# Performance work log

Hardware: AMD Instinct MI355X
Metric: run time of the kernel (lower is better)

Reference implementation:

```python
import jax, jax.numpy as jnp
import numpy as np

N, M, D = 8192, 8192, 64


def setup_inputs() -> dict:
    key = jax.random.key(0)
    k1, k2 = jax.random.split(key)
    return {
        "x": jax.random.normal(k1, (N, D), dtype=jnp.float32),
        "y": jax.random.normal(k2, (M, D), dtype=jnp.float32),
        "log_lengthscale": jnp.zeros((D,), dtype=jnp.float32),
        "log_outputscale": jnp.zeros((1,), dtype=jnp.float32),
    }


def reference(x, y, log_lengthscale, log_outputscale):
    # ARD RBF: k(x,y) = outputscale * exp(-0.5 * sum_d ((x_d - y_d)/l_d)^2)
    lengthscale = jnp.exp(log_lengthscale)          # [D]
    outputscale = jnp.exp(log_outputscale)          # [1]
    xs = x / lengthscale                            # [N, D]
    ys = y / lengthscale                            # [M, D]
    # ||xs - ys||^2 = ||xs||^2 + ||ys||^2 - 2 xs.ys^T  (GEMM rewrite, same math)
    x2 = jnp.sum(xs * xs, axis=-1)                  # [N]
    y2 = jnp.sum(ys * ys, axis=-1)                  # [M]
    cross = jnp.einsum("nd,md->nm", xs, ys)         # [N, M]
    sq_dist = jnp.maximum(x2[:, None] + y2[None, :] - 2.0 * cross, 0.0)
    return outputscale * jnp.exp(-0.5 * sq_dist)    # [N, M]
```

## Files before the change

kernel.cpp:

```cpp
#include <hip/hip_runtime.h>
#include <hip/hip_bf16.h>

#define NROWS 8192
#define MCOLS 8192
#define DDIM  64

typedef __attribute__((ext_vector_type(8))) short bf16x8;
typedef __attribute__((ext_vector_type(4))) float f32x4;
typedef __attribute__((ext_vector_type(2))) unsigned int u32x2;
typedef __attribute__((ext_vector_type(4))) unsigned int u32x4;

#define WS_NEED (4ull * 1024 * 1024 + 64 * 1024)

__global__ __launch_bounds__(256)
void pack_kernel(const float* __restrict__ x, const float* __restrict__ y,
                 const float* __restrict__ log_l, unsigned char* __restrict__ ws)
{
    const int t = threadIdx.x, lane = t & 63, wid = t >> 6;
    const int sub = lane & 15, lg = lane >> 4;
    const int gb  = blockIdx.x;
    const int isY = gb >> 7;
    const int rb  = ((gb & 127) << 2) | wid;

    const float* __restrict__ src = isY ? y : x;
    bf16x8* __restrict__ Ph = reinterpret_cast<bf16x8*>(ws + (isY ? (2u << 20) : 0u));
    bf16x8* __restrict__ Pl = reinterpret_cast<bf16x8*>(ws + (isY ? (3u << 20) : (1u << 20)));
    float*  __restrict__ nrm = reinterpret_cast<float*>(ws + (4u << 20) + (isY ? (32u << 10) : 0u));

    const int row = rb * 16 + sub;
    float psum = 0.0f;
    #pragma unroll
    for (int kk = 0; kk < 2; ++kk) {
        const int k0 = kk * 32 + lg * 8;
        f32x4 v0 = *reinterpret_cast<const f32x4*>(&src[(size_t)row * DDIM + k0]);
        f32x4 v1 = *reinterpret_cast<const f32x4*>(&src[(size_t)row * DDIM + k0 + 4]);
        f32x4 g0 = *reinterpret_cast<const f32x4*>(&log_l[k0]);
        f32x4 g1 = *reinterpret_cast<const f32x4*>(&log_l[k0 + 4]);
        float s[8];
        #pragma unroll
        for (int j = 0; j < 4; ++j) s[j]     = v0[j] * __expf(-g0[j]);
        #pragma unroll
        for (int j = 0; j < 4; ++j) s[4 + j] = v1[j] * __expf(-g1[j]);
        unsigned int hp[4], lp[4];
        #pragma unroll
        for (int p = 0; p < 4; ++p) {
            float a = s[2 * p], b = s[2 * p + 1];
            psum += a * a + b * b;
            unsigned int ua = __float_as_uint(a), ub = __float_as_uint(b);
            float la = a - __uint_as_float(ua & 0xFFFF0000u);
            float lb = b - __uint_as_float(ub & 0xFFFF0000u);
            hp[p] = (ua >> 16) | (ub & 0xFFFF0000u);
            lp[p] = ((__float_as_uint(la) + 0x8000u) >> 16) |
                    ((__float_as_uint(lb) + 0x8000u) & 0xFFFF0000u);
        }
        const int fi = (rb * 2 + kk) * 64 + lane;
        *reinterpret_cast<u32x4*>(&Ph[fi]) = u32x4{hp[0], hp[1], hp[2], hp[3]};
        *reinterpret_cast<u32x4*>(&Pl[fi]) = u32x4{lp[0], lp[1], lp[2], lp[3]};
    }
    psum += __shfl_xor(psum, 16);
    psum += __shfl_xor(psum, 32);
    if (lg == 0) nrm[row] = psum;
}

__global__ __launch_bounds__(256, 4)
void ard_rbf_main(const unsigned char* __restrict__ ws,
                  const float* __restrict__ log_os, float* __restrict__ out)
{
    __shared__ float lds[4][32][68];

    const int t = threadIdx.x, lane = t & 63, wid = t >> 6;
    const int sub = lane & 15, lg = lane >> 4;
    const int bx = blockIdx.x;
    const int by = blockIdx.y;

    const bf16x8* __restrict__ Xh = reinterpret_cast<const bf16x8*>(ws);
    const bf16x8* __restrict__ Xl = reinterpret_cast<const bf16x8*>(ws + (1u << 20));
    const bf16x8* __restrict__ Yh = reinterpret_cast<const bf16x8*>(ws + (2u << 20));
    const bf16x8* __restrict__ Yl = reinterpret_cast<const bf16x8*>(ws + (3u << 20));
    const float*  __restrict__ x2 = reinterpret_cast<const float*>(ws + (4u << 20));
    const float*  __restrict__ y2 = reinterpret_cast<const float*>(ws + (4u << 20) + (32u << 10));

    const int xrb = by * 8 + wid * 2;
    const int yrb = bx * 4;

    f32x4 acc[2][4] = {};
    #pragma unroll
    for (int kk = 0; kk < 2; ++kk) {
        bf16x8 xh[2], xl[2], yh[4], yl[4];
        #pragma unroll
        for (int a = 0; a < 2; ++a) {
            const int fi = ((xrb + a) * 2 + kk) * 64 + lane;
            xh[a] = Xh[fi];
            xl[a] = Xl[fi];
        }
        #pragma unroll
        for (int b = 0; b < 4; ++b) {
            const int fj = ((yrb + b) * 2 + kk) * 64 + lane;
            yh[b] = Yh[fj];
            yl[b] = Yl[fj];
        }
        #pragma unroll
        for (int a = 0; a < 2; ++a)
            #pragma unroll
            for (int b = 0; b < 4; ++b) {
                acc[a][b] = __builtin_amdgcn_mfma_f32_16x16x32_bf16(yh[b], xh[a], acc[a][b], 0, 0, 0);
                acc[a][b] = __builtin_amdgcn_mfma_f32_16x16x32_bf16(yl[b], xh[a], acc[a][b], 0, 0, 0);
                acc[a][b] = __builtin_amdgcn_mfma_f32_16x16x32_bf16(yh[b], xl[a], acc[a][b], 0, 0, 0);
            }
    }

    #pragma unroll
    for (int a = 0; a < 2; ++a)
        #pragma unroll
        for (int b = 0; b < 4; ++b)
            *reinterpret_cast<f32x4*>(&lds[wid][a * 16 + sub][b * 16 + lg * 4]) = acc[a][b];

    const float lnos = log_os[0];
    const int xbase = by * 128 + wid * 32;
    const int ybase = bx * 64;
    const f32x4 y2q = *reinterpret_cast<const f32x4*>(&y2[ybase + sub * 4]);

    #pragma unroll
    for (int r = 0; r < 8; ++r) {
        const int rloc = r * 4 + lg;
        f32x4 c = *reinterpret_cast<const f32x4*>(&lds[wid][rloc][sub * 4]);
        const float xs = x2[xbase + rloc];
        f32x4 v;
        #pragma unroll
        for (int j = 0; j < 4; ++j) {
            float sq = fmaxf(xs + y2q[j] - 2.0f * c[j], 0.0f);
            v[j] = __expf(fmaf(-0.5f, sq, lnos));
        }
        *reinterpret_cast<f32x4*>(out + (size_t)(xbase + rloc) * MCOLS + ybase + sub * 4) = v;
    }
}

__global__ __launch_bounds__(512, 4)
void ard_rbf_fallback(const float* __restrict__ x, const float* __restrict__ y,
                      const float* __restrict__ log_l, const float* __restrict__ log_os,
                      float* __restrict__ out)
{
    __shared__ unsigned short Ah[128][DDIM + 8], Al[128][DDIM + 8];
    __shared__ unsigned short Bh[128][DDIM + 8], Bl[128][DDIM + 8];
    __shared__ float x2s[128], y2s[128];
    __shared__ float invl[DDIM];

    const int t = threadIdx.x;
    const int bx = blockIdx.x, by = blockIdx.y;
    const int lane = t & 63, sub = lane & 15, lg = lane >> 4;

    if (t < DDIM) invl[t] = __expf(-log_l[t]);
    __syncthreads();

    #pragma unroll
    for (int ab = 0; ab < 2; ++ab) {
        const float* __restrict__ src = ab ? y : x;
        unsigned short (*Hh)[DDIM + 8] = ab ? Bh : Ah;
        unsigned short (*Hl)[DDIM + 8] = ab ? Bl : Al;
        float* nrm = ab ? y2s : x2s;
        const int tb = (ab ? bx : by) * 128;
        #pragma unroll
        for (int i = 0; i < 4; ++i) {
            const int f = i * 512 + t;
            const int row = f >> 4;
            const int c4 = (f & 15) * 4;
            f32x4 v = *reinterpret_cast<const f32x4*>(&src[(size_t)(tb + row) * DDIM + c4]);
            f32x4 il = *reinterpret_cast<const f32x4*>(&invl[c4]);
            float s0 = v[0] * il[0], s1 = v[1] * il[1], s2 = v[2] * il[2], s3 = v[3] * il[3];
            float psum = s0 * s0 + s1 * s1 + s2 * s2 + s3 * s3;
            unsigned int u0 = __float_as_uint(s0), u1 = __float_as_uint(s1);
            unsigned int u2 = __float_as_uint(s2), u3 = __float_as_uint(s3);
            float l0 = s0 - __uint_as_float(u0 & 0xFFFF0000u);
            float l1 = s1 - __uint_as_float(u1 & 0xFFFF0000u);
            float l2 = s2 - __uint_as_float(u2 & 0xFFFF0000u);
            float l3 = s3 - __uint_as_float(u3 & 0xFFFF0000u);
            unsigned int hp0 = (u0 >> 16) | (u1 & 0xFFFF0000u);
            unsigned int hp1 = (u2 >> 16) | (u3 & 0xFFFF0000u);
            unsigned int lp0 = ((__float_as_uint(l0) + 0x8000u) >> 16) | ((__float_as_uint(l1) + 0x8000u) & 0xFFFF0000u);
            unsigned int lp1 = ((__float_as_uint(l2) + 0x8000u) >> 16) | ((__float_as_uint(l3) + 0x8000u) & 0xFFFF0000u);
            psum += __shfl_xor(psum, 1);
            psum += __shfl_xor(psum, 2);
            psum += __shfl_xor(psum, 4);
            psum += __shfl_xor(psum, 8);
            *reinterpret_cast<u32x2*>(&Hh[row][c4]) = u32x2{hp0, hp1};
            *reinterpret_cast<u32x2*>(&Hl[row][c4]) = u32x2{lp0, lp1};
            if (sub == 0) nrm[row] = psum;
        }
    }
    __syncthreads();

    const int wid = t >> 6;
    const int wr = wid >> 2, wc = wid & 3;
    f32x4 acc[4][2] = {};
    #pragma unroll
    for (int kk = 0; kk < 2; ++kk) {
        const int kb = kk * 32 + lg * 8;
        bf16x8 ah[4], al[4];
        #pragma unroll
        for (int m = 0; m < 4; ++m) {
            const int r = wr * 64 + m * 16 + sub;
            ah[m] = *reinterpret_cast<const bf16x8*>(&Ah[r][kb]);
            al[m] = *reinterpret_cast<const bf16x8*>(&Al[r][kb]);
        }
        #pragma unroll
        for (int n = 0; n < 2; ++n) {
            const int c = wc * 32 + n * 16 + sub;
            bf16x8 bh = *reinterpret_cast<const bf16x8*>(&Bh[c][kb]);
            bf16x8 bl = *reinterpret_cast<const bf16x8*>(&Bl[c][kb]);
            #pragma unroll
            for (int m = 0; m < 4; ++m) {
                acc[m][n] = __builtin_amdgcn_mfma_f32_16x16x32_bf16(ah[m], bh, acc[m][n], 0, 0, 0);
                acc[m][n] = __builtin_amdgcn_mfma_f32_16x16x32_bf16(al[m], bh, acc[m][n], 0, 0, 0);
                acc[m][n] = __builtin_amdgcn_mfma_f32_16x16x32_bf16(ah[m], bl, acc[m][n], 0, 0, 0);
            }
        }
    }
    const float lnos = log_os[0];
    #pragma unroll
    for (int m = 0; m < 4; ++m) {
        const int rl0 = wr * 64 + m * 16 + lg * 4;
        #pragma unroll
        for (int n = 0; n < 2; ++n) {
            const int cl = wc * 32 + n * 16 + sub;
            const float yy2 = y2s[cl];
            const size_t g0 = (size_t)(by * 128 + rl0) * MCOLS + (size_t)(bx * 128 + cl);
            #pragma unroll
            for (int j = 0; j < 4; ++j) {
                float sq = fmaxf(x2s[rl0 + j] + yy2 - 2.0f * acc[m][n][j], 0.0f);
                out[g0 + (size_t)j * MCOLS] = __expf(fmaf(-0.5f, sq, lnos));
            }
        }
    }
}

extern "C" void kernel_launch(void* const* d_in, const int* in_sizes, int n_in,
                              void* d_out, int out_size, void* d_ws, size_t ws_size,
                              hipStream_t stream) {
    const float* x      = (const float*)d_in[0];
    const float* y      = (const float*)d_in[1];
    const float* log_l  = (const float*)d_in[2];
    const float* log_os = (const float*)d_in[3];
    float* out = (float*)d_out;

    if (ws_size >= WS_NEED) {
        pack_kernel<<<256, 256, 0, stream>>>(x, y, log_l, (unsigned char*)d_ws);
        ard_rbf_main<<<dim3(128, 64), 256, 0, stream>>>((const unsigned char*)d_ws, log_os, out);
    } else {
        ard_rbf_fallback<<<dim3(64, 64), 512, 0, stream>>>(x, y, log_l, log_os, out);
    }
}
```

Before: 63.17 us.

## Stage Y tile in LDS via global_load_lds and loop over four X tiles per block

```diff
diff --git a/kernel.cpp b/kernel.cpp
--- a/kernel.cpp
+++ b/kernel.cpp
@@ -11,6 +11,12 @@
 typedef __attribute__((ext_vector_type(4))) unsigned int u32x4;
 
 #define WS_NEED (4ull * 1024 * 1024 + 64 * 1024)
+
+__device__ __forceinline__ void gld_lds16(const unsigned char* g, unsigned char* l) {
+    __builtin_amdgcn_global_load_lds(
+        (const __attribute__((address_space(1))) void*)g,
+        (__attribute__((address_space(3))) void*)l, 16, 0, 0);
+}
 
 __global__ __launch_bounds__(256)
 void pack_kernel(const float* __restrict__ x, const float* __restrict__ y,
@@ -62,76 +68,86 @@
     if (lg == 0) nrm[row] = psum;
 }
 
-__global__ __launch_bounds__(256, 4)
+__global__ __launch_bounds__(256, 3)
 void ard_rbf_main(const unsigned char* __restrict__ ws,
                   const float* __restrict__ log_os, float* __restrict__ out)
 {
-    __shared__ float lds[4][32][68];
+    __shared__ __align__(1024) unsigned char smemY[16 * 1024];
+    __shared__ float tr[4][16][68];
 
     const int t = threadIdx.x, lane = t & 63, wid = t >> 6;
     const int sub = lane & 15, lg = lane >> 4;
     const int bx = blockIdx.x;
-    const int by = blockIdx.y;
+    const int g  = blockIdx.y;
 
     const bf16x8* __restrict__ Xh = reinterpret_cast<const bf16x8*>(ws);
     const bf16x8* __restrict__ Xl = reinterpret_cast<const bf16x8*>(ws + (1u << 20));
-    const bf16x8* __restrict__ Yh = reinterpret_cast<const bf16x8*>(ws + (2u << 20));
-    const bf16x8* __restrict__ Yl = reinterpret_cast<const bf16x8*>(ws + (3u << 20));
     const float*  __restrict__ x2 = reinterpret_cast<const float*>(ws + (4u << 20));
     const float*  __restrict__ y2 = reinterpret_cast<const float*>(ws + (4u << 20) + (32u << 10));
 
-    const int xrb = by * 8 + wid * 2;
-    const int yrb = bx * 4;
-
-    f32x4 acc[2][4] = {};
-    #pragma unroll
-    for (int kk = 0; kk < 2; ++kk) {
-        bf16x8 xh[2], xl[2], yh[4], yl[4];
-        #pragma unroll
-        for (int a = 0; a < 2; ++a) {
-            const int fi = ((xrb + a) * 2 + kk) * 64 + lane;
-            xh[a] = Xh[fi];
-            xl[a] = Xl[fi];
-        }
-        #pragma unroll
-        for (int b = 0; b < 4; ++b) {
-            const int fj = ((yrb + b) * 2 + kk) * 64 + lane;
-            yh[b] = Yh[fj];
-            yl[b] = Yl[fj];
-        }
-        #pragma unroll
-        for (int a = 0; a < 2; ++a)
-            #pragma unroll
-            for (int b = 0; b < 4; ++b) {
-                acc[a][b] = __builtin_amdgcn_mfma_f32_16x16x32_bf16(yh[b], xh[a], acc[a][b], 0, 0, 0);
-                acc[a][b] = __builtin_amdgcn_mfma_f32_16x16x32_bf16(yl[b], xh[a], acc[a][b], 0, 0, 0);
-                acc[a][b] = __builtin_amdgcn_mfma_f32_16x16x32_bf16(yh[b], xl[a], acc[a][b], 0, 0, 0);
-            }
-    }
-
-    #pragma unroll
-    for (int a = 0; a < 2; ++a)
-        #pragma unroll
-        for (int b = 0; b < 4; ++b)
-            *reinterpret_cast<f32x4*>(&lds[wid][a * 16 + sub][b * 16 + lg * 4]) = acc[a][b];
+    #pragma unroll
+    for (int i = 0; i < 4; ++i) {
+        const int c = wid * 4 + i;
+        const int fry = c >> 2, kk = (c >> 1) & 1, hl = c & 1;
+        const size_t goff = (2u << 20) + ((size_t)hl << 20)
+                          + ((size_t)((((bx * 4 + fry) * 2 + kk) * 64 + lane)) << 4);
+        gld_lds16(ws + goff, smemY + c * 1024);
+    }
+    __syncthreads();
 
     const float lnos = log_os[0];
-    const int xbase = by * 128 + wid * 32;
     const int ybase = bx * 64;
     const f32x4 y2q = *reinterpret_cast<const f32x4*>(&y2[ybase + sub * 4]);
 
     #pragma unroll
-    for (int r = 0; r < 8; ++r) {
-        const int rloc = r * 4 + lg;
-        f32x4 c = *reinterpret_cast<const f32x4*>(&lds[wid][rloc][sub * 4]);
-        const float xs = x2[xbase + rloc];
-        f32x4 v;
-        #pragma unroll
-        for (int j = 0; j < 4; ++j) {
-            float sq = fmaxf(xs + y2q[j] - 2.0f * c[j], 0.0f);
-            v[j] = __expf(fmaf(-0.5f, sq, lnos));
-        }
-        *reinterpret_cast<f32x4*>(out + (size_t)(xbase + rloc) * MCOLS + ybase + sub * 4) = v;
+    for (int it = 0; it < 4; ++it) {
+        const int by = g * 4 + it;
+
+        f32x4 acc[2][4] = {};
+        #pragma unroll
+        for (int kk = 0; kk < 2; ++kk) {
+            bf16x8 xh[2], xl[2], yh[4], yl[4];
+            #pragma unroll
+            for (int a = 0; a < 2; ++a) {
+                const int fi = ((by * 8 + wid * 2 + a) * 2 + kk) * 64 + lane;
+                xh[a] = Xh[fi];
+                xl[a] = Xl[fi];
+            }
+            #pragma unroll
+            for (int b = 0; b < 4; ++b) {
+                yh[b] = *reinterpret_cast<const bf16x8*>(smemY + (b * 4 + kk * 2 + 0) * 1024 + lane * 16);
+                yl[b] = *reinterpret_cast<const bf16x8*>(smemY + (b * 4 + kk * 2 + 1) * 1024 + lane * 16);
+            }
+            #pragma unroll
+            for (int a = 0; a < 2; ++a)
+                #pragma unroll
+                for (int b = 0; b < 4; ++b) {
+                    acc[a][b] = __builtin_amdgcn_mfma_f32_16x16x32_bf16(yh[b], xh[a], acc[a][b], 0, 0, 0);
+                    acc[a][b] = __builtin_amdgcn_mfma_f32_16x16x32_bf16(yl[b], xh[a], acc[a][b], 0, 0, 0);
+                    acc[a][b] = __builtin_amdgcn_mfma_f32_16x16x32_bf16(yh[b], xl[a], acc[a][b], 0, 0, 0);
+                }
+        }
+
+        #pragma unroll
+        for (int a = 0; a < 2; ++a) {
+            #pragma unroll
+            for (int b = 0; b < 4; ++b)
+                *reinterpret_cast<f32x4*>(&tr[wid][sub][b * 16 + lg * 4]) = acc[a][b];
+            const int xb = by * 128 + wid * 32 + a * 16;
+            #pragma unroll
+            for (int r = 0; r < 4; ++r) {
+                const int rl = r * 4 + lg;
+                f32x4 c = *reinterpret_cast<const f32x4*>(&tr[wid][rl][sub * 4]);
+                const float xs = x2[xb + rl];
+                f32x4 v;
+                #pragma unroll
+                for (int j = 0; j < 4; ++j) {
+                    float sq = fmaxf(xs + y2q[j] - 2.0f * c[j], 0.0f);
+                    v[j] = __expf(fmaf(-0.5f, sq, lnos));
+                }
+                *reinterpret_cast<f32x4*>(out + (size_t)(xb + rl) * MCOLS + ybase + sub * 4) = v;
+            }
+        }
     }
 }
 
@@ -244,7 +260,7 @@
 
     if (ws_size >= WS_NEED) {
         pack_kernel<<<256, 256, 0, stream>>>(x, y, log_l, (unsigned char*)d_ws);
-        ard_rbf_main<<<dim3(128, 64), 256, 0, stream>>>((const unsigned char*)d_ws, log_os, out);
+        ard_rbf_main<<<dim3(128, 16), 256, 0, stream>>>((const unsigned char*)d_ws, log_os, out);
     } else {
         ard_rbf_fallback<<<dim3(64, 64), 512, 0, stream>>>(x, y, log_l, log_os, out);
     }
```

Result: faster. 56.54 us (-10.5%).
